# Performance work log

Measured on AMD Instinct MI355X. Metric: run time of the kernel, lower is better.

## Reference

```python
import jax, jax.numpy as jnp
import numpy as np

# Static geometry (derived from calc_block_params for H=W=1024, bcount=32, k=3, s=1)
B, H, W, C = 1, 1024, 1024, 64
COUT, K, STRIDE = 64, 3, 1
BC = 32      # block count per spatial dim
BS = 34      # gather block size (bsize)
BSTR = 32    # block stride (bsize - k + stride)
BOUT = 32    # conv output block size (bsize_out)
NACT = 512
PAD = 1      # pad each side (total pad = 2 per dim)


def setup_inputs() -> dict:
    key = jax.random.key(0)
    k1, k2, k3, k4 = jax.random.split(key, 4)
    x = jax.random.normal(k1, (B, H, W, C), jnp.float32)
    # unique active block ids (flat b*BC*BC + i*BC + j), like gen_reducemask's randperm
    block_ids = jax.random.permutation(k2, B * BC * BC)[:NACT].astype(jnp.int32)
    Wk = jax.random.normal(k3, (K, K, C, COUT), jnp.float32) * 0.05
    bias = jax.random.normal(k4, (COUT,), jnp.float32) * 0.05
    return {"x": x, "block_ids": block_ids, "Wk": Wk, "bias": bias}


def _gather_blocks(xp, bidx, iidx, jidx):
    # sparse_gather: slice [BS,BS,C] block at (b, i*BSTR, j*BSTR) from padded input
    def one(bi, ii, jj):
        return jax.lax.dynamic_slice(xp, (bi, ii * BSTR, jj * BSTR, 0), (1, BS, BS, C))[0]
    return jax.vmap(one)(bidx, iidx, jidx)  # [NACT, BS, BS, C]


def reference(x, block_ids, Wk, bias):
    # F.pad with padding_params (0,0,pl,pr,pt,pb) on NHWC -> pad H and W by 1 each side
    xp = jnp.pad(x, ((0, 0), (PAD, PAD), (PAD, PAD), (0, 0)))
    bidx = block_ids // (BC * BC)
    iidx = (block_ids // BC) % BC
    jidx = block_ids % BC
    p = _gather_blocks(xp, bidx, iidx, jidx)  # [NACT, BS, BS, C]
    # dense conv on stacked active blocks (VALID, stride 1): [NACT, BOUT, BOUT, COUT]
    q = jax.lax.conv_general_dilated(
        p, Wk, window_strides=(STRIDE, STRIDE), padding='VALID',
        dimension_numbers=('NHWC', 'HWIO', 'NHWC')) + bias
    # sparse_scatter with bstride = bsize_out: non-overlapping tiling -> set semantics
    out_blocks = jnp.zeros((B * BC * BC, BOUT, BOUT, COUT), q.dtype).at[block_ids].set(q)
    y = out_blocks.reshape(B, BC, BC, BOUT, BOUT, COUT)
    y = y.transpose(0, 1, 3, 2, 4, 5).reshape(B, BC * BOUT, BC * BOUT, COUT)
    return y  # [1, 1024, 1024, 64]
```

## Files before the change

kernel.cpp:

```cpp
#include <hip/hip_runtime.h>
#include <hip/hip_bf16.h>
#include <stdint.h>


typedef __bf16 bf16x8 __attribute__((ext_vector_type(8)));
typedef float f32x16 __attribute__((ext_vector_type(16)));
typedef float f32x4 __attribute__((ext_vector_type(4)));

#define WFRAG_BYTES 73728
#define FLAGS_OFF   WFRAG_BYTES
#define INACT_OFF   (FLAGS_OFF + 4096)
#define CNT_OFF     (INACT_OFF + 2048)

__device__ __forceinline__ unsigned f2bf1(float f) {
    unsigned u = __float_as_uint(f);
    u += 0x7fffu + ((u >> 16) & 1u);
    return u >> 16;
}
__device__ __forceinline__ unsigned pack2(float lo, float hi) {
    return f2bf1(lo) | (f2bf1(hi) << 16);
}

__global__ __launch_bounds__(256) void k_prep(const float* __restrict__ Wk,
                                              const int* __restrict__ ids,
                                              unsigned short* __restrict__ wfrag,
                                              int* __restrict__ flags,
                                              int* __restrict__ inact,
                                              int* __restrict__ cnt) {
    int tid = threadIdx.x;
    if (blockIdx.x == 18) {
        #pragma unroll
        for (int i = 0; i < 4; ++i) flags[tid * 4 + i] = 0;
        if (tid == 0) cnt[0] = 0;
        __syncthreads();
        flags[ids[tid]] = 1;
        flags[ids[tid + 256]] = 1;
        __syncthreads();
        #pragma unroll
        for (int i = 0; i < 4; ++i) {
            int b = tid * 4 + i;
            if (flags[b] == 0) {
                int pos = atomicAdd(cnt, 1);
                inact[pos] = b;
            }
        }
        return;
    }
    int t = blockIdx.x * 256 + tid;
    int lane = t & 63;
    int nt   = (t >> 6) & 1;
    int s    = (t >> 7) & 3;
    int tap  = t >> 9;
    int co = nt * 32 + (lane & 31);
    int cb = s * 16 + 8 * (lane >> 5);
    const float* wp = Wk + (tap * 64 + cb) * 64 + co;
    uint4 v;
    v.x = pack2(wp[0],   wp[64]);
    v.y = pack2(wp[128], wp[192]);
    v.z = pack2(wp[256], wp[320]);
    v.w = pack2(wp[384], wp[448]);
    ((uint4*)wfrag)[t] = v;
}

__global__ __launch_bounds__(512, 4) void k_conv(
    const float* __restrict__ x, const float* __restrict__ bias,
    const uint4* __restrict__ wfrag, const int* __restrict__ ids,
    const int* __restrict__ inact, float* __restrict__ out)
{
    __shared__ __align__(16) char lds[10 * 34 * 128];
    const int w = blockIdx.x;
    const int u = ((w & 7) << 8) | (w >> 3);
    const int li = u >> 2, p = u & 3;
    const int tid = threadIdx.x;

    {
        const int zb = inact[li];
        const int zbi = zb >> 5, zbj = zb & 31;
        const f32x4 z = {0.f, 0.f, 0.f, 0.f};
        #pragma unroll
        for (int py = 0; py < 8; ++py) {
            f32x4* rowp = (f32x4*)(out + ((zbi * 32 + p * 8 + py) * 1024 + zbj * 32) * 64);
            __builtin_nontemporal_store(z, rowp + tid);
        }
    }

    const int bid = ids[li];
    const int bi = bid >> 5, bj = bid & 31;
    const int lane = tid & 63;
    const int wv = tid >> 6;

    float4 ra[3][4];
    int rbase[3];
    int rswz[3];
    #pragma unroll
    for (int k = 0; k < 3; ++k) {
        int uu = tid + k * 512;
        bool live = (k < 2) || (tid < 336);
        int q   = uu & 3;
        int pix = uu >> 2;
        int ly  = pix / 34;
        int lx  = pix - ly * 34;
        int yg = bi * 32 + p * 8 - 1 + ly;
        int xg = bj * 32 - 1 + lx;
        rbase[k] = pix * 128 + q * 32;
        rswz[k]  = (lx & 7) << 4;
        ra[k][0] = make_float4(0.f, 0.f, 0.f, 0.f);
        ra[k][1] = make_float4(0.f, 0.f, 0.f, 0.f);
        ra[k][2] = make_float4(0.f, 0.f, 0.f, 0.f);
        ra[k][3] = make_float4(0.f, 0.f, 0.f, 0.f);
        if (live && (unsigned)yg < 1024u && (unsigned)xg < 1024u) {
            const float4* gp = (const float4*)(x + ((yg * 1024 + xg) * 64 + q * 16));
            ra[k][0] = gp[0]; ra[k][1] = gp[1]; ra[k][2] = gp[2]; ra[k][3] = gp[3];
        }
        if (!live) rbase[k] = -1;
    }
    #pragma unroll
    for (int k = 0; k < 3; ++k) {
        if (rbase[k] < 0) continue;
        bf16x8 v0, v1;
        float4 a = ra[k][0], b = ra[k][1], c = ra[k][2], d = ra[k][3];
        v0[0] = (__bf16)a.x; v0[1] = (__bf16)a.y; v0[2] = (__bf16)a.z; v0[3] = (__bf16)a.w;
        v0[4] = (__bf16)b.x; v0[5] = (__bf16)b.y; v0[6] = (__bf16)b.z; v0[7] = (__bf16)b.w;
        v1[0] = (__bf16)c.x; v1[1] = (__bf16)c.y; v1[2] = (__bf16)c.z; v1[3] = (__bf16)c.w;
        v1[4] = (__bf16)d.x; v1[5] = (__bf16)d.y; v1[6] = (__bf16)d.z; v1[7] = (__bf16)d.w;
        *(bf16x8*)(lds + (rbase[k] ^ rswz[k]))        = v0;
        *(bf16x8*)(lds + ((rbase[k] + 16) ^ rswz[k])) = v1;
    }
    __syncthreads();

    const float b0 = bias[lane & 31];
    const float b1 = bias[32 + (lane & 31)];
    f32x16 acc0, acc1;
    #pragma unroll
    for (int r = 0; r < 16; ++r) { acc0[r] = b0; acc1[r] = b1; }

    const int xl = lane & 31;
    const int chalf = 16 * (lane >> 5);

    #pragma unroll
    for (int kx = 0; kx < 3; ++kx) {
        int xp = xl + kx;
        int swz = (xp & 7) << 4;
        #pragma unroll
        for (int s = 0; s < 4; ++s) {
            int cbyte = s * 32 + chalf;
            bf16x8 a0 = *(const bf16x8*)(lds + ((((wv + 0) * 34 + xp) * 128 + cbyte) ^ swz));
            bf16x8 a1 = *(const bf16x8*)(lds + ((((wv + 1) * 34 + xp) * 128 + cbyte) ^ swz));
            bf16x8 a2 = *(const bf16x8*)(lds + ((((wv + 2) * 34 + xp) * 128 + cbyte) ^ swz));
            #pragma unroll
            for (int ky = 0; ky < 3; ++ky) {
                int fi = ((ky * 3 + kx) * 8 + s * 2) * 64 + lane;
                bf16x8 bf0 = *(const bf16x8*)(wfrag + fi);
                bf16x8 bf1 = *(const bf16x8*)(wfrag + fi + 64);
                bf16x8 a = (ky == 0) ? a0 : (ky == 1) ? a1 : a2;
                acc0 = __builtin_amdgcn_mfma_f32_32x32x16_bf16(a, bf0, acc0, 0, 0, 0);
                acc1 = __builtin_amdgcn_mfma_f32_32x32x16_bf16(a, bf1, acc1, 0, 0, 0);
            }
        }
    }

    const int row = bi * 32 + p * 8 + wv;
    float* orow = out + (row * 1024 + bj * 32) * 64;
    const int co = lane & 31;
    #pragma unroll
    for (int r = 0; r < 16; ++r) {
        int px = (r & 3) + 8 * (r >> 2) + 4 * (lane >> 5);
        __builtin_nontemporal_store(acc0[r], orow + px * 64 + co);
        __builtin_nontemporal_store(acc1[r], orow + px * 64 + co + 32);
    }
}

extern "C" void kernel_launch(void* const* d_in, const int* in_sizes, int n_in,
                              void* d_out, int out_size, void* d_ws, size_t ws_size,
                              hipStream_t stream) {
    const float* x    = (const float*)d_in[0];
    const int*   ids  = (const int*)d_in[1];
    const float* Wk   = (const float*)d_in[2];
    const float* bias = (const float*)d_in[3];
    float* out = (float*)d_out;

    unsigned short* wfrag = (unsigned short*)d_ws;
    int* flags = (int*)((char*)d_ws + FLAGS_OFF);
    int* inact = (int*)((char*)d_ws + INACT_OFF);
    int* cnt   = (int*)((char*)d_ws + CNT_OFF);

    k_prep<<<19, 256, 0, stream>>>(Wk, ids, wfrag, flags, inact, cnt);
    k_conv<<<2048, 512, 0, stream>>>(x, bias, (const uint4*)wfrag, ids, inact, out);
}
```

Measured before the change: 82.08 us.

## Compute two output rows per wave with 16-row halo tiles and half the workgroups

Each workgroup now handles 16 output rows of a block instead of 8, and each wave computes two adjacent rows. The wave reuses four loaded A rows and the weight fragments across both rows, so the halo overhead falls from 10/8 to 18/16 and fewer weight loads are needed per MFMA. The grid halves to 1024 workgroups and LDS per workgroup grows to about 78KB. That limits occupancy and doubles accumulator registers, and the staging loop is no longer fully unrolled.

```diff
diff --git a/kernel.cpp b/kernel.cpp
--- a/kernel.cpp
+++ b/kernel.cpp
@@ -67,10 +67,10 @@
     const uint4* __restrict__ wfrag, const int* __restrict__ ids,
     const int* __restrict__ inact, float* __restrict__ out)
 {
-    __shared__ __align__(16) char lds[10 * 34 * 128];
+    __shared__ __align__(16) char lds[18 * 34 * 128];
     const int w = blockIdx.x;
-    const int u = ((w & 7) << 8) | (w >> 3);
-    const int li = u >> 2, p = u & 3;
+    const int u = ((w & 7) << 7) | (w >> 3);
+    const int li = u >> 1, p = u & 1;
     const int tid = threadIdx.x;
 
     {
@@ -78,8 +78,8 @@
         const int zbi = zb >> 5, zbj = zb & 31;
         const f32x4 z = {0.f, 0.f, 0.f, 0.f};
         #pragma unroll
-        for (int py = 0; py < 8; ++py) {
-            f32x4* rowp = (f32x4*)(out + ((zbi * 32 + p * 8 + py) * 1024 + zbj * 32) * 64);
+        for (int py = 0; py < 16; ++py) {
+            f32x4* rowp = (f32x4*)(out + ((zbi * 32 + p * 16 + py) * 1024 + zbj * 32) * 64);
             __builtin_nontemporal_store(z, rowp + tid);
         }
     }
@@ -89,50 +89,36 @@
     const int lane = tid & 63;
     const int wv = tid >> 6;
 
-    float4 ra[3][4];
-    int rbase[3];
-    int rswz[3];
-    #pragma unroll
-    for (int k = 0; k < 3; ++k) {
-        int uu = tid + k * 512;
-        bool live = (k < 2) || (tid < 336);
-        int q   = uu & 3;
-        int pix = uu >> 2;
+    for (int t = tid; t < 18 * 34 * 4; t += 512) {
+        int q   = t & 3;
+        int pix = t >> 2;
         int ly  = pix / 34;
         int lx  = pix - ly * 34;
-        int yg = bi * 32 + p * 8 - 1 + ly;
+        int yg = bi * 32 + p * 16 - 1 + ly;
         int xg = bj * 32 - 1 + lx;
-        rbase[k] = pix * 128 + q * 32;
-        rswz[k]  = (lx & 7) << 4;
-        ra[k][0] = make_float4(0.f, 0.f, 0.f, 0.f);
-        ra[k][1] = make_float4(0.f, 0.f, 0.f, 0.f);
-        ra[k][2] = make_float4(0.f, 0.f, 0.f, 0.f);
-        ra[k][3] = make_float4(0.f, 0.f, 0.f, 0.f);
-        if (live && (unsigned)yg < 1024u && (unsigned)xg < 1024u) {
+        bf16x8 v0 = {}, v1 = {};
+        if ((unsigned)yg < 1024u && (unsigned)xg < 1024u) {
             const float4* gp = (const float4*)(x + ((yg * 1024 + xg) * 64 + q * 16));
-            ra[k][0] = gp[0]; ra[k][1] = gp[1]; ra[k][2] = gp[2]; ra[k][3] = gp[3];
+            float4 a = gp[0], b = gp[1], c = gp[2], d = gp[3];
+            v0[0] = (__bf16)a.x; v0[1] = (__bf16)a.y; v0[2] = (__bf16)a.z; v0[3] = (__bf16)a.w;
+            v0[4] = (__bf16)b.x; v0[5] = (__bf16)b.y; v0[6] = (__bf16)b.z; v0[7] = (__bf16)b.w;
+            v1[0] = (__bf16)c.x; v1[1] = (__bf16)c.y; v1[2] = (__bf16)c.z; v1[3] = (__bf16)c.w;
+            v1[4] = (__bf16)d.x; v1[5] = (__bf16)d.y; v1[6] = (__bf16)d.z; v1[7] = (__bf16)d.w;
         }
-        if (!live) rbase[k] = -1;
-    }
-    #pragma unroll
-    for (int k = 0; k < 3; ++k) {
-        if (rbase[k] < 0) continue;
-        bf16x8 v0, v1;
-        float4 a = ra[k][0], b = ra[k][1], c = ra[k][2], d = ra[k][3];
-        v0[0] = (__bf16)a.x; v0[1] = (__bf16)a.y; v0[2] = (__bf16)a.z; v0[3] = (__bf16)a.w;
-        v0[4] = (__bf16)b.x; v0[5] = (__bf16)b.y; v0[6] = (__bf16)b.z; v0[7] = (__bf16)b.w;
-        v1[0] = (__bf16)c.x; v1[1] = (__bf16)c.y; v1[2] = (__bf16)c.z; v1[3] = (__bf16)c.w;
-        v1[4] = (__bf16)d.x; v1[5] = (__bf16)d.y; v1[6] = (__bf16)d.z; v1[7] = (__bf16)d.w;
-        *(bf16x8*)(lds + (rbase[k] ^ rswz[k]))        = v0;
-        *(bf16x8*)(lds + ((rbase[k] + 16) ^ rswz[k])) = v1;
+        int base = pix * 128 + q * 32;
+        int swz  = (lx & 7) << 4;
+        *(bf16x8*)(lds + (base ^ swz))        = v0;
+        *(bf16x8*)(lds + ((base + 16) ^ swz)) = v1;
     }
     __syncthreads();
 
     const float b0 = bias[lane & 31];
     const float b1 = bias[32 + (lane & 31)];
-    f32x16 acc0, acc1;
+    f32x16 acc[2][2];
     #pragma unroll
-    for (int r = 0; r < 16; ++r) { acc0[r] = b0; acc1[r] = b1; }
+    for (int dm = 0; dm < 2; ++dm)
+        #pragma unroll
+        for (int r = 0; r < 16; ++r) { acc[dm][0][r] = b0; acc[dm][1][r] = b1; }
 
     const int xl = lane & 31;
     const int chalf = 16 * (lane >> 5);
@@ -144,29 +130,36 @@
         #pragma unroll
         for (int s = 0; s < 4; ++s) {
             int cbyte = s * 32 + chalf;
-            bf16x8 a0 = *(const bf16x8*)(lds + ((((wv + 0) * 34 + xp) * 128 + cbyte) ^ swz));
-            bf16x8 a1 = *(const bf16x8*)(lds + ((((wv + 1) * 34 + xp) * 128 + cbyte) ^ swz));
-            bf16x8 a2 = *(const bf16x8*)(lds + ((((wv + 2) * 34 + xp) * 128 + cbyte) ^ swz));
+            bf16x8 a0 = *(const bf16x8*)(lds + ((((2 * wv + 0) * 34 + xp) * 128 + cbyte) ^ swz));
+            bf16x8 a1 = *(const bf16x8*)(lds + ((((2 * wv + 1) * 34 + xp) * 128 + cbyte) ^ swz));
+            bf16x8 a2 = *(const bf16x8*)(lds + ((((2 * wv + 2) * 34 + xp) * 128 + cbyte) ^ swz));
+            bf16x8 a3 = *(const bf16x8*)(lds + ((((2 * wv + 3) * 34 + xp) * 128 + cbyte) ^ swz));
             #pragma unroll
             for (int ky = 0; ky < 3; ++ky) {
                 int fi = ((ky * 3 + kx) * 8 + s * 2) * 64 + lane;
                 bf16x8 bf0 = *(const bf16x8*)(wfrag + fi);
                 bf16x8 bf1 = *(const bf16x8*)(wfrag + fi + 64);
-                bf16x8 a = (ky == 0) ? a0 : (ky == 1) ? a1 : a2;
-                acc0 = __builtin_amdgcn_mfma_f32_32x32x16_bf16(a, bf0, acc0, 0, 0, 0);
-                acc1 = __builtin_amdgcn_mfma_f32_32x32x16_bf16(a, bf1, acc1, 0, 0, 0);
+                bf16x8 ar0 = (ky == 0) ? a0 : (ky == 1) ? a1 : a2;
+                bf16x8 ar1 = (ky == 0) ? a1 : (ky == 1) ? a2 : a3;
+                acc[0][0] = __builtin_amdgcn_mfma_f32_32x32x16_bf16(ar0, bf0, acc[0][0], 0, 0, 0);
+                acc[0][1] = __builtin_amdgcn_mfma_f32_32x32x16_bf16(ar0, bf1, acc[0][1], 0, 0, 0);
+                acc[1][0] = __builtin_amdgcn_mfma_f32_32x32x16_bf16(ar1, bf0, acc[1][0], 0, 0, 0);
+                acc[1][1] = __builtin_amdgcn_mfma_f32_32x32x16_bf16(ar1, bf1, acc[1][1], 0, 0, 0);
             }
         }
     }
 
-    const int row = bi * 32 + p * 8 + wv;
-    float* orow = out + (row * 1024 + bj * 32) * 64;
     const int co = lane & 31;
     #pragma unroll
-    for (int r = 0; r < 16; ++r) {
-        int px = (r & 3) + 8 * (r >> 2) + 4 * (lane >> 5);
-        __builtin_nontemporal_store(acc0[r], orow + px * 64 + co);
-        __builtin_nontemporal_store(acc1[r], orow + px * 64 + co + 32);
+    for (int dm = 0; dm < 2; ++dm) {
+        int row = bi * 32 + p * 16 + 2 * wv + dm;
+        float* orow = out + (row * 1024 + bj * 32) * 64;
+        #pragma unroll
+        for (int r = 0; r < 16; ++r) {
+            int px = (r & 3) + 8 * (r >> 2) + 4 * (lane >> 5);
+            __builtin_nontemporal_store(acc[dm][0][r], orow + px * 64 + co);
+            __builtin_nontemporal_store(acc[dm][1][r], orow + px * 64 + co + 32);
+        }
     }
 }
 
@@ -185,5 +178,5 @@
     int* cnt   = (int*)((char*)d_ws + CNT_OFF);
 
     k_prep<<<19, 256, 0, stream>>>(Wk, ids, wfrag, flags, inact, cnt);
-    k_conv<<<2048, 512, 0, stream>>>(x, bias, (const uint4*)wfrag, ids, inact, out);
+    k_conv<<<1024, 512, 0, stream>>>(x, bias, (const uint4*)wfrag, ids, inact, out);
 }
```

Result: faster. 79.51 us (-3.1%).
